# Kernel tuning notes

Hardware: AMD Instinct MI355X
Metric: run time of the kernel (lower is better)

The kernel has to match this reference:

```python
import jax, jax.numpy as jnp
import numpy as np

BN_EPS = 1e-5


def setup_inputs() -> dict:
    key = jax.random.key(0)
    ks = jax.random.split(key, 6)
    B, C, N, K, T, O = 8, 64, 4096, 20, 3, 64
    feat = jax.random.normal(ks[0], (B, C, N), dtype=jnp.float32)
    idx = jax.random.randint(ks[1], (B, N, K), 0, N, dtype=jnp.int32)
    group_pc = jax.random.normal(ks[2], (B, 3, N, K), dtype=jnp.float32)
    weights = jax.random.normal(ks[3], (B, 20, T, N, K), dtype=jnp.float32) * 0.05
    conv_w = jax.random.normal(ks[4], (O, C * T, K), dtype=jnp.float32) * 0.02
    gamma = jnp.ones((O,), dtype=jnp.float32)
    beta = jnp.zeros((O,), dtype=jnp.float32)
    return {"feat": feat, "idx": idx, "group_pc": group_pc, "weights": weights,
            "conv_w": conv_w, "gamma": gamma, "beta": beta}


def _poly_terms(group_pc):
    # group_pc: (B, 3, N, K) -> 20 Taylor terms (B, 20, N, K)
    X, Y, Z = group_pc[:, 0], group_pc[:, 1], group_pc[:, 2]
    XX, YY, ZZ = X * X, Y * Y, Z * Z
    XY, XZ, YZ = X * Y, X * Z, Y * Z
    ones = jnp.ones_like(X)
    return jnp.stack([
        ones, X, Y, Z,
        XX, YY, ZZ,
        XX * X, YY * Y, ZZ * Z,
        XY, XZ, YZ,
        X * XY, X * XZ, Y * YZ, Y * XY, Z * XZ, Z * YZ, XY * Z,
    ], axis=1)


def reference(feat, idx, group_pc, weights, conv_w, gamma, beta):
    B, C, N = feat.shape
    K = idx.shape[-1]
    T = weights.shape[2]
    # KNN gather: group_feat[b, c, n, j] = feat[b, c, idx[b, n, j]]  -> (B, C, N, K)
    group_feat = jax.vmap(lambda f, i: f[:, i])(feat, idx)
    # 20 polynomial basis terms of XYZ: (B, 20, N, K)
    terms = _poly_terms(group_pc)
    # taylor[b, t, n, k] = sum_p weights[b, p, t, n, k] * terms[b, p, n, k]
    taylor = jnp.einsum('bptnk,bpnk->btnk', weights, terms)
    # Fused outer-product + [1, K] conv (output width 1, no bias since bn=True):
    # out[b, o, n] = sum_{c, t, k} group_feat[b,c,n,k] * taylor[b,t,n,k] * W[o, c*T+t, k]
    w = conv_w.reshape(conv_w.shape[0], C, T, K)
    out = jnp.einsum('bcnk,btnk,octk->bon', group_feat, taylor, w)
    # BatchNorm (training-mode batch stats over B and N) + ReLU
    mean = jnp.mean(out, axis=(0, 2), keepdims=True)
    var = jnp.var(out, axis=(0, 2), keepdims=True)
    out = gamma[None, :, None] * (out - mean) / jnp.sqrt(var + BN_EPS) + beta[None, :, None]
    return jax.nn.relu(out)
```

## Files before the change

kernel.cpp:

```cpp
#include <hip/hip_runtime.h>
#include <hip/hip_bf16.h>

#define B_ 8
#define C_ 64
#define N_ 4096
#define K_ 20
#define T_ 3
#define O_ 64
#define P_ 20
#define NK_ (N_ * K_)
#define BN_EPS 1e-5f

#define WS_FEATT 0
#define WS_WT (WS_FEATT + B_ * N_ * C_)
#define WS_RAW (WS_WT + 122880)
#define WS_PART (WS_RAW + B_ * O_ * N_)
#define WS_STATS (WS_PART + 131072)

typedef __attribute__((ext_vector_type(8))) _Float16 half8;
typedef __attribute__((ext_vector_type(2))) _Float16 half2v;
typedef __attribute__((ext_vector_type(2))) __fp16 fp16x2;
typedef __attribute__((ext_vector_type(16))) float f32x16;

union UH8 {
    uint4 u;
    half8 h;
    half2v h2[4];
};
union UH2 {
    unsigned u;
    half2v h;
    fp16x2 f;
};

__device__ inline unsigned cvt_pkrtz_u(float a, float b) {
    UH2 x;
    x.f = __builtin_amdgcn_cvt_pkrtz(a, b);
    return x.u;
}

__global__ void k_transpose_feat(const float* __restrict__ feat, float* __restrict__ featT) {
    __shared__ float t[64][65];
    int bid = blockIdx.x;
    int b = bid & 7;
    int n0 = (bid >> 3) << 6;
    int lx = threadIdx.x & 63, ly = threadIdx.x >> 6;
    const float* fp = feat + b * C_ * N_;
#pragma unroll
    for (int cc = 0; cc < 16; ++cc) {
        int c = ly * 16 + cc;
        t[c][lx] = fp[c * N_ + n0 + lx];
    }
    __syncthreads();
    float* op = featT + (b * N_ + n0) * C_;
#pragma unroll
    for (int u = 0; u < 16; ++u) {
        int n = ly * 16 + u;
        op[n * C_ + lx] = t[lx][n];
    }
}

__global__ void k_pack_w(const float* __restrict__ cw, _Float16* __restrict__ Wh) {
    int e = blockIdx.x * 256 + threadIdx.x;
    int j = e & 7;
    int l = (e >> 3) & 63;
    int frag = e >> 9;
    int oh = frag & 1;
    int cc = (frag >> 1) & 3;
    int kt = frag >> 3;
    int t = kt % 3, k = kt / 3;
    int o = oh * 32 + (l & 31);
    int c = cc * 16 + (l >> 5) * 8 + j;
    Wh[e] = (_Float16)cw[o * (C_ * T_ * K_) + (c * T_ + t) * K_ + k];
}

__global__ __launch_bounds__(512, 8) void k_main(const float* __restrict__ featT,
                                                 const _Float16* __restrict__ Wh,
                                                 const float* __restrict__ weights,
                                                 const float* __restrict__ gpc,
                                                 const int* __restrict__ idx,
                                                 float* __restrict__ raw,
                                                 float* __restrict__ part) {
    __shared__ unsigned short Gh[2][32][72];
    __shared__ union {
        struct {
            unsigned tayH[T_][K_][32];
            int idxS[K_][32];
        } s;
        float out[64][36];
    } su;

    const int bid0 = blockIdx.x;
    const int bid = (bid0 & 7) * 128 + (bid0 >> 3);
    const int b = bid >> 7;
    const int n0 = (bid & 127) << 5;
    const int tid = threadIdx.x;
    const int lane = tid & 63;
    const int wv = tid >> 6;
    const int wc = wv & 3;
    const int wo = wv >> 2;
    const int nl = lane & 31;
    const int kf = lane >> 5;

    {
        const int* ip = idx + (b * N_ + n0) * K_;
        for (int e = tid; e < 32 * K_; e += 512) su.s.idxS[e % K_][e / K_] = ip[e];
    }
    {
        const float* gpcb = gpc + (size_t)b * 3 * NK_ + n0 * K_;
        const float* wb0 = weights + (size_t)b * P_ * T_ * NK_ + n0 * K_;
        for (int e = tid; e < 32 * K_; e += 512) {
            float X = gpcb[e];
            float Y = gpcb[NK_ + e];
            float Z = gpcb[2 * NK_ + e];
            float XX = X * X, YY = Y * Y, ZZ = Z * Z;
            float XY = X * Y, XZ = X * Z, YZ = Y * Z;
            float terms[20];
            terms[0] = 1.f; terms[1] = X;      terms[2] = Y;       terms[3] = Z;
            terms[4] = XX;  terms[5] = YY;     terms[6] = ZZ;
            terms[7] = XX * X; terms[8] = YY * Y; terms[9] = ZZ * Z;
            terms[10] = XY; terms[11] = XZ;    terms[12] = YZ;
            terms[13] = X * XY;
            terms[14] = X * XZ;
            terms[15] = Y * YZ;
            terms[16] = Y * XY;
            terms[17] = Z * XZ;
            terms[18] = Z * YZ;
            terms[19] = XY * Z;
            float a0 = 0.f, a1 = 0.f, a2 = 0.f;
            const float* wp = wb0 + e;
#pragma unroll
            for (int p = 0; p < P_; ++p) {
                float tp = terms[p];
                a0 += wp[0] * tp;
                a1 += wp[(size_t)NK_] * tp;
                a2 += wp[2 * (size_t)NK_] * tp;
                wp += 3 * (size_t)NK_;
            }
            int n = e / K_, k = e - (e / K_) * K_;
            su.s.tayH[0][k][n] = cvt_pkrtz_u(a0, a0);
            su.s.tayH[1][k][n] = cvt_pkrtz_u(a1, a1);
            su.s.tayH[2][k][n] = cvt_pkrtz_u(a2, a2);
        }
    }
    __syncthreads();

    f32x16 acc;
#pragma unroll
    for (int i = 0; i < 16; ++i) acc[i] = 0.f;

    const float* fb = featT + (size_t)b * N_ * C_;
    const int r = tid >> 4, sseg = tid & 15;

    float4 st = *(const float4*)(fb + su.s.idxS[0][r] * C_ + sseg * 4);

    for (int k = 0; k < K_; ++k) {
        const int buf = k & 1;
        uint2 w;
        w.x = cvt_pkrtz_u(st.x, st.y);
        w.y = cvt_pkrtz_u(st.z, st.w);
        *(uint2*)&Gh[buf][r][sseg * 4] = w;
        __syncthreads();
        if (k + 1 < K_) {
            st = *(const float4*)(fb + su.s.idxS[k + 1][r] * C_ + sseg * 4);
        }
        UH8 g;
        g.u = *(const uint4*)&Gh[buf][nl][wc * 16 + kf * 8];
#pragma unroll
        for (int t = 0; t < 3; ++t) {
            UH8 ar;
            ar.u = *(const uint4*)(Wh +
                                   (size_t)((((k * 3 + t) * 4 + wc) * 2 + wo) * 64 + lane) * 8);
            UH2 tv;
            tv.u = su.s.tayH[t][k][nl];
            UH8 bv;
#pragma unroll
            for (int i = 0; i < 4; ++i) bv.h2[i] = g.h2[i] * tv.h;
            acc = __builtin_amdgcn_mfma_f32_32x32x16_f16(ar.h, bv.h, acc, 0, 0, 0);
        }
    }

    __syncthreads();
#pragma unroll 1
    for (int ww = 0; ww < 4; ++ww) {
        if (wc == ww) {
#pragma unroll
            for (int rr = 0; rr < 16; ++rr) {
                int row = wo * 32 + (rr & 3) + ((rr >> 2) << 3) + (kf << 2);
                if (ww == 0)
                    su.out[row][nl] = acc[rr];
                else
                    su.out[row][nl] += acc[rr];
            }
        }
        __syncthreads();
    }

    {
        int o = tid >> 3, seg = tid & 7;
        float4* dst = (float4*)(raw + ((b * O_ + o) * N_) + n0 + seg * 4);
        const float* srow = &su.out[o][seg * 4];
        *dst = make_float4(srow[0], srow[1], srow[2], srow[3]);
    }
    if (tid < 64) {
        float s1 = 0.f, s2 = 0.f;
#pragma unroll 8
        for (int n = 0; n < 32; ++n) {
            float v = su.out[tid][n];
            s1 += v;
            s2 += v * v;
        }
        part[(bid * 64 + tid) * 2 + 0] = s1;
        part[(bid * 64 + tid) * 2 + 1] = s2;
    }
}

__global__ void k_bnstats(const float* __restrict__ part, const float* __restrict__ gamma,
                          const float* __restrict__ beta, float* __restrict__ stats) {
    int o = blockIdx.x;
    int tid = threadIdx.x;
    __shared__ float s1s[256], s2s[256];
    float s1 = 0.f, s2 = 0.f;
    for (int j = tid; j < 1024; j += 256) {
        s1 += part[(j * 64 + o) * 2 + 0];
        s2 += part[(j * 64 + o) * 2 + 1];
    }
    s1s[tid] = s1;
    s2s[tid] = s2;
    __syncthreads();
    for (int s = 128; s > 0; s >>= 1) {
        if (tid < s) {
            s1s[tid] += s1s[tid + s];
            s2s[tid] += s2s[tid + s];
        }
        __syncthreads();
    }
    if (tid == 0) {
        const float cnt = (float)(B_ * N_);
        float mean = s1s[0] / cnt;
        float var = s2s[0] / cnt - mean * mean;
        float sc = gamma[o] * rsqrtf(var + BN_EPS);
        stats[o * 2 + 0] = sc;
        stats[o * 2 + 1] = beta[o] - mean * sc;
    }
}

__global__ void k_finalize(const float* __restrict__ raw, const float* __restrict__ stats,
                           float* __restrict__ out) {
    int e = (blockIdx.x * 256 + threadIdx.x) * 4;
    int o = (e >> 12) & 63;
    float sc = stats[o * 2 + 0], sh = stats[o * 2 + 1];
    float4 v = *(const float4*)(raw + e);
    v.x = fmaxf(v.x * sc + sh, 0.f);
    v.y = fmaxf(v.y * sc + sh, 0.f);
    v.z = fmaxf(v.z * sc + sh, 0.f);
    v.w = fmaxf(v.w * sc + sh, 0.f);
    *(float4*)(out + e) = v;
}

extern "C" void kernel_launch(void* const* d_in, const int* in_sizes, int n_in,
                              void* d_out, int out_size, void* d_ws, size_t ws_size,
                              hipStream_t stream) {
    const float* feat = (const float*)d_in[0];
    const int* idx = (const int*)d_in[1];
    const float* gpc = (const float*)d_in[2];
    const float* weights = (const float*)d_in[3];
    const float* conv_w = (const float*)d_in[4];
    const float* gamma = (const float*)d_in[5];
    const float* beta = (const float*)d_in[6];
    float* out = (float*)d_out;
    float* ws = (float*)d_ws;

    float* featT = ws + WS_FEATT;
    _Float16* Wh = (_Float16*)(ws + WS_WT);
    float* raw = ws + WS_RAW;
    float* part = ws + WS_PART;
    float* stats = ws + WS_STATS;

    hipLaunchKernelGGL(k_transpose_feat, dim3(512), dim3(256), 0, stream, feat, featT);
    hipLaunchKernelGGL(k_pack_w, dim3((K_ * T_ * C_ * O_) / 256), dim3(256), 0, stream, conv_w,
                       Wh);
    hipLaunchKernelGGL(k_main, dim3(B_ * (N_ / 32)), dim3(512), 0, stream, featT, Wh, weights,
                       gpc, idx, raw, part);
    hipLaunchKernelGGL(k_bnstats, dim3(O_), dim3(256), 0, stream, part, gamma, beta, stats);
    hipLaunchKernelGGL(k_finalize, dim3(B_ * O_ * N_ / 4 / 256), dim3(256), 0, stream, raw, stats,
                       out);
}
```

Before: 78.22 us.

## Batch KNN feature gathers in groups of five with register double-buffering

Restructures the main MFMA loop so that neighbor feature rows are gathered five at a time into registers, two groups ahead, and staged into a double-buffered shared tile. This cuts block-wide barriers from one per neighbor to one per group. Gather indices are now loaded straight into registers with int4 loads instead of through shared memory, and the first gathers are issued before the Taylor-weight computation so their latency overlaps it. It raises register pressure, so launch bounds are relaxed from 8 to 4 blocks per multiprocessor, which may reduce occupancy.

```diff
diff --git a/kernel.cpp b/kernel.cpp
--- a/kernel.cpp
+++ b/kernel.cpp
@@ -10,6 +10,7 @@
 #define P_ 20
 #define NK_ (N_ * K_)
 #define BN_EPS 1e-5f
+#define KG 5
 
 #define WS_FEATT 0
 #define WS_WT (WS_FEATT + B_ * N_ * C_)
@@ -74,19 +75,16 @@
     Wh[e] = (_Float16)cw[o * (C_ * T_ * K_) + (c * T_ + t) * K_ + k];
 }
 
-__global__ __launch_bounds__(512, 8) void k_main(const float* __restrict__ featT,
+__global__ __launch_bounds__(512, 4) void k_main(const float* __restrict__ featT,
                                                  const _Float16* __restrict__ Wh,
                                                  const float* __restrict__ weights,
                                                  const float* __restrict__ gpc,
                                                  const int* __restrict__ idx,
                                                  float* __restrict__ raw,
                                                  float* __restrict__ part) {
-    __shared__ unsigned short Gh[2][32][72];
+    __shared__ unsigned short E[2][KG][32][68];
     __shared__ union {
-        struct {
-            unsigned tayH[T_][K_][32];
-            int idxS[K_][32];
-        } s;
+        unsigned tayH[T_][K_][32];
         float out[64][36];
     } su;
 
@@ -101,11 +99,28 @@
     const int wo = wv >> 2;
     const int nl = lane & 31;
     const int kf = lane >> 5;
-
+    const int row = tid >> 4, seg = tid & 15;
+
+    const float* fb = featT + (size_t)b * N_ * C_;
+
+    int idxv[K_];
     {
-        const int* ip = idx + (b * N_ + n0) * K_;
-        for (int e = tid; e < 32 * K_; e += 512) su.s.idxS[e % K_][e / K_] = ip[e];
-    }
+        const int4* ip4 = (const int4*)(idx + (size_t)(b * N_ + n0 + row) * K_);
+#pragma unroll
+        for (int q = 0; q < 5; ++q) {
+            int4 v = ip4[q];
+            idxv[q * 4 + 0] = v.x;
+            idxv[q * 4 + 1] = v.y;
+            idxv[q * 4 + 2] = v.z;
+            idxv[q * 4 + 3] = v.w;
+        }
+    }
+
+    float4 gA[KG], gB[KG];
+#pragma unroll
+    for (int kk = 0; kk < KG; ++kk)
+        gA[kk] = *(const float4*)(fb + (size_t)idxv[kk] * C_ + seg * 4);
+
     {
         const float* gpcb = gpc + (size_t)b * 3 * NK_ + n0 * K_;
         const float* wb0 = weights + (size_t)b * P_ * T_ * NK_ + n0 * K_;
@@ -137,69 +152,88 @@
                 a2 += wp[2 * (size_t)NK_] * tp;
                 wp += 3 * (size_t)NK_;
             }
-            int n = e / K_, k = e - (e / K_) * K_;
-            su.s.tayH[0][k][n] = cvt_pkrtz_u(a0, a0);
-            su.s.tayH[1][k][n] = cvt_pkrtz_u(a1, a1);
-            su.s.tayH[2][k][n] = cvt_pkrtz_u(a2, a2);
-        }
-    }
+            int n = e / K_, k = e - n * K_;
+            su.tayH[0][k][n] = cvt_pkrtz_u(a0, a0);
+            su.tayH[1][k][n] = cvt_pkrtz_u(a1, a1);
+            su.tayH[2][k][n] = cvt_pkrtz_u(a2, a2);
+        }
+    }
+
+#pragma unroll
+    for (int kk = 0; kk < KG; ++kk) {
+        uint2 w;
+        w.x = cvt_pkrtz_u(gA[kk].x, gA[kk].y);
+        w.y = cvt_pkrtz_u(gA[kk].z, gA[kk].w);
+        *(uint2*)&E[0][kk][row][seg * 4] = w;
+    }
+#pragma unroll
+    for (int kk = 0; kk < KG; ++kk)
+        gA[kk] = *(const float4*)(fb + (size_t)idxv[KG + kk] * C_ + seg * 4);
     __syncthreads();
 
     f32x16 acc;
 #pragma unroll
     for (int i = 0; i < 16; ++i) acc[i] = 0.f;
 
-    const float* fb = featT + (size_t)b * N_ * C_;
-    const int r = tid >> 4, sseg = tid & 15;
-
-    float4 st = *(const float4*)(fb + su.s.idxS[0][r] * C_ + sseg * 4);
-
-    for (int k = 0; k < K_; ++k) {
-        const int buf = k & 1;
-        uint2 w;
-        w.x = cvt_pkrtz_u(st.x, st.y);
-        w.y = cvt_pkrtz_u(st.z, st.w);
-        *(uint2*)&Gh[buf][r][sseg * 4] = w;
+#pragma unroll
+    for (int p = 0; p < 4; ++p) {
+        if (p + 2 < 4) {
+#pragma unroll
+            for (int kk = 0; kk < KG; ++kk) {
+                float4 v = *(const float4*)(fb + (size_t)idxv[(p + 2) * KG + kk] * C_ + seg * 4);
+                if (p & 1) gA[kk] = v; else gB[kk] = v;
+            }
+        }
+#pragma unroll
+        for (int kk = 0; kk < KG; ++kk) {
+            UH8 gv;
+            gv.u = *(const uint4*)&E[p & 1][kk][nl][wc * 16 + kf * 8];
+            const int k = p * KG + kk;
+#pragma unroll
+            for (int t = 0; t < 3; ++t) {
+                UH8 ar;
+                ar.u = *(const uint4*)(Wh +
+                                       (size_t)((((k * 3 + t) * 4 + wc) * 2 + wo) * 64 + lane) * 8);
+                UH2 tv;
+                tv.u = su.tayH[t][k][nl];
+                UH8 bv;
+#pragma unroll
+                for (int i = 0; i < 4; ++i) bv.h2[i] = gv.h2[i] * tv.h;
+                acc = __builtin_amdgcn_mfma_f32_32x32x16_f16(ar.h, bv.h, acc, 0, 0, 0);
+            }
+        }
+        if (p + 1 < 4) {
+#pragma unroll
+            for (int kk = 0; kk < KG; ++kk) {
+                float4 v = (p & 1) ? gB[kk] : gA[kk];
+                uint2 w;
+                w.x = cvt_pkrtz_u(v.x, v.y);
+                w.y = cvt_pkrtz_u(v.z, v.w);
+                *(uint2*)&E[(p + 1) & 1][kk][row][seg * 4] = w;
+            }
+        }
         __syncthreads();
-        if (k + 1 < K_) {
-            st = *(const float4*)(fb + su.s.idxS[k + 1][r] * C_ + sseg * 4);
-        }
-        UH8 g;
-        g.u = *(const uint4*)&Gh[buf][nl][wc * 16 + kf * 8];
-#pragma unroll
-        for (int t = 0; t < 3; ++t) {
-            UH8 ar;
-            ar.u = *(const uint4*)(Wh +
-                                   (size_t)((((k * 3 + t) * 4 + wc) * 2 + wo) * 64 + lane) * 8);
-            UH2 tv;
-            tv.u = su.s.tayH[t][k][nl];
-            UH8 bv;
-#pragma unroll
-            for (int i = 0; i < 4; ++i) bv.h2[i] = g.h2[i] * tv.h;
-            acc = __builtin_amdgcn_mfma_f32_32x32x16_f16(ar.h, bv.h, acc, 0, 0, 0);
-        }
-    }
-
-    __syncthreads();
+    }
+
 #pragma unroll 1
     for (int ww = 0; ww < 4; ++ww) {
         if (wc == ww) {
 #pragma unroll
             for (int rr = 0; rr < 16; ++rr) {
-                int row = wo * 32 + (rr & 3) + ((rr >> 2) << 3) + (kf << 2);
+                int orow = wo * 32 + (rr & 3) + ((rr >> 2) << 3) + (kf << 2);
                 if (ww == 0)
-                    su.out[row][nl] = acc[rr];
+                    su.out[orow][nl] = acc[rr];
                 else
-                    su.out[row][nl] += acc[rr];
+                    su.out[orow][nl] += acc[rr];
             }
         }
         __syncthreads();
     }
 
     {
-        int o = tid >> 3, seg = tid & 7;
-        float4* dst = (float4*)(raw + ((b * O_ + o) * N_) + n0 + seg * 4);
-        const float* srow = &su.out[o][seg * 4];
+        int o = tid >> 3, sg = tid & 7;
+        float4* dst = (float4*)(raw + ((b * O_ + o) * N_) + n0 + sg * 4);
+        const float* srow = &su.out[o][sg * 4];
         *dst = make_float4(srow[0], srow[1], srow[2], srow[3]);
     }
     if (tid < 64) {
```

Result: faster. 70.67 us (-9.7%).
